# Kernel tuning notes

Measured on AMD Instinct MI355X. Metric: run time of the kernel, lower is better.

## Reference

```python
import jax, jax.numpy as jnp
import numpy as np

K_MASK = -2.3819763e38  # gemma masking constant


def apply_rope(inputs, positions, head_dim):
    # inputs: [B, T, N, H], positions: [B, T]
    half = head_dim // 2
    fraction = 2.0 * jnp.arange(half, dtype=jnp.float32) / head_dim
    timescale = 10000.0 ** fraction                      # [half]
    sinusoid = positions[..., None].astype(jnp.float32) / timescale  # [B, T, half]
    sin = jnp.sin(sinusoid)[:, :, None, :]               # [B, T, 1, half]
    cos = jnp.cos(sinusoid)[:, :, None, :]
    first, second = jnp.split(inputs, 2, axis=-1)
    out = jnp.concatenate([first * cos - second * sin,
                           second * cos + first * sin], axis=-1)
    return out.astype(inputs.dtype)


def setup_inputs() -> dict:
    key = jax.random.key(0)
    k0, k1, k2, k3 = jax.random.split(key, 4)
    B, T, D, N, H = 4, 1024, 2048, 16, 128
    x = jax.random.normal(k0, (B, T, D), dtype=jnp.float32)
    wq = jax.random.normal(k1, (N, D, H), dtype=jnp.float32) * 0.02
    wkv = jax.random.normal(k2, (2, 1, D, H), dtype=jnp.float32) * 0.02  # MQA: 1 kv head
    wo = jax.random.normal(k3, (N, H, D), dtype=jnp.float32) * 0.02
    segment_pos = jnp.broadcast_to(jnp.arange(T, dtype=jnp.int32), (B, T))
    attn_mask = jnp.broadcast_to(jnp.tril(jnp.ones((T, T), dtype=bool)), (B, T, T))
    return {"x": x, "wq": wq, "wkv": wkv, "wo": wo,
            "segment_pos": segment_pos, "attn_mask": attn_mask}


def reference(x, wq, wkv, wo, segment_pos, attn_mask):
    N, _, H = wq.shape
    # projections
    q = jnp.einsum('BTD,NDH->BTNH', x, wq)          # [B,T,N,H]
    kv = jnp.einsum('BSD,CKDH->CBSKH', x, wkv)      # [2,B,S,1,H]
    k, v = kv[0], kv[1]
    # RoPE + scaling
    q = apply_rope(q, segment_pos, H) * (H ** -0.5)
    k = apply_rope(k, segment_pos, H)
    # MQA head repeat: 1 kv head -> N heads
    k = jnp.repeat(k, N, axis=-2)                   # [B,S,N,H]
    v = jnp.repeat(v, N, axis=-2)
    # attention with manual masked softmax
    logits = jnp.einsum('BTNH,BSNH->BTNS', q, k)
    padded = jnp.where(attn_mask[:, :, None, :], logits, K_MASK)
    probs = jax.nn.softmax(padded, axis=-1).astype(k.dtype)
    encoded = jnp.einsum('BTNS,BSNH->BTNH', probs, v)
    return jnp.einsum('BTNH,NHD->BTD', encoded, wo)
```

## Files before the change

kernel.cpp:

```cpp
#include <hip/hip_runtime.h>
#include <cstdint>
#include <cstddef>

typedef unsigned short u16;
typedef __attribute__((ext_vector_type(8))) short bf16x8;
typedef __attribute__((ext_vector_type(4))) float f32x4;

#define B_ 4
#define T_ 1024
#define D_ 2048
#define N_ 16
#define H_ 128
#define BT_ (B_ * T_)
#define KMASK (-2.3819763e38f)

__device__ __forceinline__ u16 f2bf(float f) {
  uint32_t u = __builtin_bit_cast(uint32_t, f);
  u += 0x7FFFu + ((u >> 16) & 1u);
  return (u16)(u >> 16);
}
__device__ __forceinline__ float bf2f(uint32_t u) {
  return __builtin_bit_cast(float, u << 16);
}

__device__ __forceinline__ void gload16(const void* g, void* l) {
  __builtin_amdgcn_global_load_lds((const __attribute__((address_space(1))) void*)g,
                                   (__attribute__((address_space(3))) void*)l, 16, 0, 0);
}

__global__ __launch_bounds__(256) void convert_x_kernel(const float* __restrict__ x,
                                                        u16* __restrict__ xb) {
  int i = (blockIdx.x * 256 + threadIdx.x) * 8;
  float4 v0 = *(const float4*)(x + i);
  float4 v1 = *(const float4*)(x + i + 4);
  uint4 o;
  o.x = (uint32_t)f2bf(v0.x) | ((uint32_t)f2bf(v0.y) << 16);
  o.y = (uint32_t)f2bf(v0.z) | ((uint32_t)f2bf(v0.w) << 16);
  o.z = (uint32_t)f2bf(v1.x) | ((uint32_t)f2bf(v1.y) << 16);
  o.w = (uint32_t)f2bf(v1.z) | ((uint32_t)f2bf(v1.w) << 16);
  *(uint4*)(xb + i) = o;
}

__global__ __launch_bounds__(256) void transpose_kernel(const float* __restrict__ src,
                                                        u16* __restrict__ dst, int R, int C) {
  __shared__ float tile[32][33];
  const int z = blockIdx.z;
  const float* s = src + (size_t)z * R * C;
  u16* d = dst + (size_t)z * R * C;
  const int tx = threadIdx.x, ty = threadIdx.y;
  const int r0 = blockIdx.y * 32, c0 = blockIdx.x * 32;
#pragma unroll
  for (int i = 0; i < 4; ++i)
    tile[ty + i * 8][tx] = s[(size_t)(r0 + ty + i * 8) * C + (c0 + tx)];
  __syncthreads();
#pragma unroll
  for (int i = 0; i < 4; ++i)
    d[(size_t)(c0 + ty + i * 8) * R + (r0 + tx)] = f2bf(tile[tx][ty + i * 8]);
}

__global__ __launch_bounds__(256) void rope_table_kernel(float* __restrict__ costab,
                                                         float* __restrict__ sintab) {
  int idx = blockIdx.x * 256 + threadIdx.x;
  int p = idx >> 6, i = idx & 63;
  float ts = powf(10000.0f, (float)i * (1.0f / 64.0f));
  float ang = (float)p / ts;
  costab[idx] = cosf(ang);
  sintab[idx] = sinf(ang);
}

__global__ __launch_bounds__(256) void proj_gemm_kernel(
    const u16* __restrict__ xb, const u16* __restrict__ wqT, const u16* __restrict__ wkvT,
    u16* __restrict__ qraw, u16* __restrict__ kraw, u16* __restrict__ vT) {
  __shared__ alignas(16) u16 a_lds[128 * 64];
  __shared__ alignas(16) u16 b_lds[128 * 64];
  const int bid = blockIdx.x;
  const int newbid = (bid & 7) * 72 + (bid >> 3);
  const int y = newbid >> 5;
  const int m0 = (newbid & 31) * 128;
  const u16* Bt = (y < N_) ? (wqT + (size_t)y * H_ * D_) : (wkvT + (size_t)(y - N_) * H_ * D_);
  const int tid = threadIdx.x;
  const int w = tid >> 6, lane = tid & 63;
  const int g = lane >> 4, li = lane & 15;
  const int mrow = (w >> 1) * 64, wc = (w & 1) * 64;
  f32x4 acc[4][4];
#pragma unroll
  for (int i = 0; i < 4; ++i)
#pragma unroll
    for (int j = 0; j < 4; ++j) acc[i][j] = (f32x4){0.f, 0.f, 0.f, 0.f};

  for (int k0 = 0; k0 < D_; k0 += 64) {
    __syncthreads();
#pragma unroll
    for (int it = 0; it < 4; ++it) {
      int chunk = it * 256 + tid;
      int row = chunk >> 3, cu = chunk & 7;
      gload16(xb + (size_t)(m0 + row) * D_ + k0 + ((cu ^ (row & 7)) << 3), &a_lds[chunk * 8]);
    }
#pragma unroll
    for (int it = 0; it < 4; ++it) {
      int chunk = it * 256 + tid;
      int row = chunk >> 3, cu = chunk & 7;
      gload16(Bt + (size_t)row * D_ + k0 + ((cu ^ (row & 7)) << 3), &b_lds[chunk * 8]);
    }
    __syncthreads();
#pragma unroll
    for (int c2 = 0; c2 < 2; ++c2) {
      bf16x8 af[4], bfr[4];
#pragma unroll
      for (int i = 0; i < 4; ++i) {
        int row = mrow + i * 16 + li;
        af[i] = *(const bf16x8*)((const char*)a_lds +
                                 row * 128 + ((c2 * 64 + g * 16) ^ ((row & 7) << 4)));
      }
#pragma unroll
      for (int j = 0; j < 4; ++j) {
        int row = wc + j * 16 + li;
        bfr[j] = *(const bf16x8*)((const char*)b_lds +
                                  row * 128 + ((c2 * 64 + g * 16) ^ ((row & 7) << 4)));
      }
#pragma unroll
      for (int i = 0; i < 4; ++i)
#pragma unroll
        for (int j = 0; j < 4; ++j)
          acc[i][j] = __builtin_amdgcn_mfma_f32_16x16x32_bf16(af[i], bfr[j], acc[i][j], 0, 0, 0);
    }
  }

  const int b = m0 >> 10;
  if (y == N_ + 1) {
    const int tbase0 = (m0 & 1023) + mrow;
#pragma unroll
    for (int i = 0; i < 4; ++i) {
      int tbase = tbase0 + i * 16 + g * 4;
#pragma unroll
      for (int j = 0; j < 4; ++j) {
        int h = wc + j * 16 + li;
        ushort4 pk;
        pk.x = f2bf(acc[i][j][0]);
        pk.y = f2bf(acc[i][j][1]);
        pk.z = f2bf(acc[i][j][2]);
        pk.w = f2bf(acc[i][j][3]);
        *(ushort4*)(vT + ((size_t)(b * H_ + h)) * T_ + tbase) = pk;
      }
    }
  } else {
    size_t rowbase = (y < N_) ? ((size_t)(b * N_ + y) * T_ + (m0 & 1023)) : (size_t)m0;
    u16* dst0 = (y < N_) ? qraw : kraw;
#pragma unroll
    for (int i = 0; i < 4; ++i)
#pragma unroll
      for (int r = 0; r < 4; ++r) {
        int trow = mrow + i * 16 + g * 4 + r;
        u16* dst = dst0 + (rowbase + trow) * H_;
#pragma unroll
        for (int j = 0; j < 4; ++j) dst[wc + j * 16 + li] = f2bf(acc[i][j][r]);
      }
  }
}

__global__ __launch_bounds__(256) void rope_apply_k_kernel(
    const u16* __restrict__ kraw, const int* __restrict__ segment_pos,
    const float* __restrict__ costab, const float* __restrict__ sintab,
    u16* __restrict__ kb) {
  const int rid = blockIdx.x * 8 + (threadIdx.x >> 5);
  const int j = threadIdx.x & 31;
  const u16* src = kraw + (size_t)rid * H_;
  u16* dst = kb + (size_t)rid * H_;
  int p = segment_pos[rid];
  p = p < 0 ? 0 : (p > 1023 ? 1023 : p);
  uint32_t ua = *(const uint32_t*)(src + 2 * j);
  uint32_t ub = *(const uint32_t*)(src + 64 + 2 * j);
  float2 cv = *(const float2*)(costab + p * 64 + 2 * j);
  float2 sv = *(const float2*)(sintab + p * 64 + 2 * j);
  float f1a = bf2f(ua & 0xffffu), f1b = bf2f(ua >> 16);
  float f2a = bf2f(ub & 0xffffu), f2b = bf2f(ub >> 16);
  *(uint32_t*)(dst + 2 * j) =
      (uint32_t)f2bf(f1a * cv.x - f2a * sv.x) | ((uint32_t)f2bf(f1b * cv.y - f2b * sv.y) << 16);
  *(uint32_t*)(dst + 64 + 2 * j) =
      (uint32_t)f2bf(f2a * cv.x + f1a * sv.x) | ((uint32_t)f2bf(f2b * cv.y + f1b * sv.y) << 16);
}

__global__ __launch_bounds__(256) void attn_kernel(
    const u16* __restrict__ qraw, const u16* __restrict__ kb, const u16* __restrict__ vT,
    const int* __restrict__ segment_pos, const float* __restrict__ costab,
    const float* __restrict__ sintab, u16* __restrict__ enc) {
  __shared__ alignas(16) u16 k_lds[2][64 * 128];
  __shared__ alignas(16) u16 v_lds[2][128 * 64];
  __shared__ alignas(16) u16 p_lds[4 * 2 * 16 * 64];
  const int bx = blockIdx.x;
  const int j = bx >> 6;
  const int bn = bx & 63;
  const int b = bn >> 4, n = bn & 15;
  const int tid = threadIdx.x, w = tid >> 6, lane = tid & 63;
  const int g = lane >> 4, li = lane & 15;
  const int t0g[2] = {j * 64 + w * 16, (15 - j) * 64 + w * 16};

  bf16x8 qf[2][4];
  const float scale = 0.08838834764831845f;
#pragma unroll
  for (int u = 0; u < 2; ++u) {
    const int trow = t0g[u] + li;
    const u16* qrow = qraw + ((size_t)(b * N_ + n) * T_ + trow) * H_;
#pragma unroll
    for (int c = 0; c < 4; ++c) qf[u][c] = *(const bf16x8*)(qrow + c * 32 + g * 8);
    int p = segment_pos[b * T_ + trow];
    p = p < 0 ? 0 : (p > 1023 ? 1023 : p);
#pragma unroll
    for (int c = 0; c < 2; ++c) {
      const float* cp = costab + p * 64 + c * 32 + g * 8;
      const float* sp = sintab + p * 64 + c * 32 + g * 8;
      f32x4 cv0 = *(const f32x4*)cp, cv1 = *(const f32x4*)(cp + 4);
      f32x4 sv0 = *(const f32x4*)sp, sv1 = *(const f32x4*)(sp + 4);
#pragma unroll
      for (int e = 0; e < 8; ++e) {
        float cvv = e < 4 ? cv0[e] : cv1[e - 4];
        float svv = e < 4 ? sv0[e] : sv1[e - 4];
        float f1 = bf2f((u16)qf[u][c][e]);
        float f2 = bf2f((u16)qf[u][c + 2][e]);
        qf[u][c][e] = (short)f2bf((f1 * cvv - f2 * svv) * scale);
        qf[u][c + 2][e] = (short)f2bf((f2 * cvv + f1 * svv) * scale);
      }
    }
  }

  f32x4 o[2][8];
#pragma unroll
  for (int u = 0; u < 2; ++u)
#pragma unroll
    for (int hn = 0; hn < 8; ++hn) o[u][hn] = (f32x4){0.f, 0.f, 0.f, 0.f};
  float m[2] = {-3e38f, -3e38f}, lsum[2] = {0.f, 0.f};

  auto stageKV = [&](int buf, int s0) {
#pragma unroll
    for (int it = 0; it < 4; ++it) {
      int chunk = it * 256 + tid;
      int row = chunk >> 4, cu = chunk & 15;
      gload16(kb + ((size_t)b * T_ + s0 + row) * H_ + ((cu ^ (row & 7)) << 3),
              &k_lds[buf][chunk * 8]);
    }
#pragma unroll
    for (int it = 0; it < 4; ++it) {
      int chunk = it * 256 + tid;
      int row = chunk >> 3, cu = chunk & 7;
      gload16(vT + ((size_t)(b * H_ + row)) * T_ + s0 + ((cu ^ (row & 7)) << 3),
              &v_lds[buf][chunk * 8]);
    }
  };

  const int nst = 16 - j;
  stageKV(0, 0);
  __syncthreads();
  int cur = 0;
  for (int st = 0; st < nst; ++st) {
    const int s0 = st * 64;
    if (st + 1 < nst) stageKV(cur ^ 1, (st + 1) * 64);
    const bool actA = (st <= j);

    f32x4 sacc[2][4];
#pragma unroll
    for (int u = 0; u < 2; ++u)
#pragma unroll
      for (int fn = 0; fn < 4; ++fn) sacc[u][fn] = (f32x4){0.f, 0.f, 0.f, 0.f};
    __builtin_amdgcn_s_setprio(1);
#pragma unroll
    for (int c = 0; c < 4; ++c) {
      bf16x8 kf[4];
#pragma unroll
      for (int fn = 0; fn < 4; ++fn) {
        int row = fn * 16 + li;
        kf[fn] = *(const bf16x8*)((const char*)&k_lds[cur][0] +
                                  row * 256 + ((c * 64 + g * 16) ^ ((row & 7) << 4)));
      }
#pragma unroll
      for (int fn = 0; fn < 4; ++fn)
        sacc[1][fn] = __builtin_amdgcn_mfma_f32_16x16x32_bf16(kf[fn], qf[1][c], sacc[1][fn], 0, 0, 0);
      if (actA)
#pragma unroll
        for (int fn = 0; fn < 4; ++fn)
          sacc[0][fn] = __builtin_amdgcn_mfma_f32_16x16x32_bf16(kf[fn], qf[0][c], sacc[0][fn], 0, 0, 0);
    }
    __builtin_amdgcn_s_setprio(0);

#pragma unroll
    for (int u = 0; u < 2; ++u) {
      if (u == 0 && !actA) continue;
      const int t0 = t0g[u];
      const bool needmask = (u == 0) ? (st == j) : (st == nst - 1);
      if (needmask) {
        int trow = t0 + li;
#pragma unroll
        for (int fn = 0; fn < 4; ++fn)
#pragma unroll
          for (int r = 0; r < 4; ++r)
            if (s0 + fn * 16 + g * 4 + r > trow) sacc[u][fn][r] = KMASK;
      }
      float mx = -3e38f;
#pragma unroll
      for (int fn = 0; fn < 4; ++fn)
#pragma unroll
        for (int r = 0; r < 4; ++r) mx = fmaxf(mx, sacc[u][fn][r]);
      mx = fmaxf(mx, __shfl_xor(mx, 16, 64));
      mx = fmaxf(mx, __shfl_xor(mx, 32, 64));
      float mn = fmaxf(m[u], mx);
      float alpha = __expf(m[u] - mn);
      m[u] = mn;
      float ps = 0.f;
#pragma unroll
      for (int fn = 0; fn < 4; ++fn)
#pragma unroll
        for (int r = 0; r < 4; ++r) {
          float p = __expf(sacc[u][fn][r] - mn);
          sacc[u][fn][r] = p;
          ps += p;
        }
      ps += __shfl_xor(ps, 16, 64);
      ps += __shfl_xor(ps, 32, 64);
      lsum[u] = lsum[u] * alpha + ps;
      char* pbase = (char*)p_lds + (w * 2 + u) * 2048;
#pragma unroll
      for (int fn = 0; fn < 4; ++fn) {
        ushort4 pk;
        pk.x = f2bf(sacc[u][fn][0]);
        pk.y = f2bf(sacc[u][fn][1]);
        pk.z = f2bf(sacc[u][fn][2]);
        pk.w = f2bf(sacc[u][fn][3]);
        *(ushort4*)(pbase + li * 128 + ((fn * 32 + g * 8) ^ ((li & 7) << 4))) = pk;
      }
#pragma unroll
      for (int r = 0; r < 4; ++r) {
        float ar = __shfl(alpha, g * 4 + r, 64);
#pragma unroll
        for (int hn = 0; hn < 8; ++hn) o[u][hn][r] *= ar;
      }
    }

    __builtin_amdgcn_s_setprio(1);
#pragma unroll
    for (int c2 = 0; c2 < 2; ++c2) {
      bf16x8 pfB = *(const bf16x8*)((char*)p_lds + (w * 2 + 1) * 2048 + li * 128 +
                                    ((c2 * 64 + g * 16) ^ ((li & 7) << 4)));
      bf16x8 pfA;
      if (actA)
        pfA = *(const bf16x8*)((char*)p_lds + (w * 2 + 0) * 2048 + li * 128 +
                               ((c2 * 64 + g * 16) ^ ((li & 7) << 4)));
#pragma unroll
      for (int hn = 0; hn < 8; ++hn) {
        int hrow = hn * 16 + li;
        bf16x8 vf = *(const bf16x8*)((const char*)&v_lds[cur][0] +
                                     hrow * 128 + ((c2 * 64 + g * 16) ^ ((li & 7) << 4)));
        o[1][hn] = __builtin_amdgcn_mfma_f32_16x16x32_bf16(pfB, vf, o[1][hn], 0, 0, 0);
        if (actA)
          o[0][hn] = __builtin_amdgcn_mfma_f32_16x16x32_bf16(pfA, vf, o[0][hn], 0, 0, 0);
      }
    }
    __builtin_amdgcn_s_setprio(0);
    __syncthreads();
    cur ^= 1;
  }

#pragma unroll
  for (int u = 0; u < 2; ++u)
#pragma unroll
    for (int r = 0; r < 4; ++r) {
      float lr = __shfl(lsum[u], g * 4 + r, 64);
      float inv = 1.0f / lr;
      int t = t0g[u] + g * 4 + r;
      u16* dst = enc + ((size_t)(b * T_ + t)) * (N_ * H_) + n * H_;
#pragma unroll
      for (int hn = 0; hn < 8; ++hn) dst[hn * 16 + li] = f2bf(o[u][hn][r] * inv);
    }
}

__global__ __launch_bounds__(256) void out_gemm_kernel(const u16* __restrict__ enc,
                                                       const u16* __restrict__ woT,
                                                       float* __restrict__ out) {
  __shared__ alignas(16) u16 a_lds[128 * 64];
  __shared__ alignas(16) u16 b_lds[128 * 64];
  const int bid = blockIdx.x;
  const int newbid = (bid & 7) * 64 + (bid >> 3);
  const int m0 = (newbid & 31) * 128;
  const int n0 = (newbid >> 5) * 128;
  const int tid = threadIdx.x, w = tid >> 6, lane = tid & 63;
  const int g = lane >> 4, li = lane & 15;
  const int mrow = (w >> 1) * 64, wc = (w & 1) * 64;
  f32x4 acc[4][4];
#pragma unroll
  for (int i = 0; i < 4; ++i)
#pragma unroll
    for (int j = 0; j < 4; ++j) acc[i][j] = (f32x4){0.f, 0.f, 0.f, 0.f};

  for (int k0 = 0; k0 < D_; k0 += 64) {
    __syncthreads();
#pragma unroll
    for (int it = 0; it < 4; ++it) {
      int chunk = it * 256 + tid;
      int row = chunk >> 3, cu = chunk & 7;
      gload16(enc + (size_t)(m0 + row) * D_ + k0 + ((cu ^ (row & 7)) << 3), &a_lds[chunk * 8]);
    }
#pragma unroll
    for (int it = 0; it < 4; ++it) {
      int chunk = it * 256 + tid;
      int row = chunk >> 3, cu = chunk & 7;
      gload16(woT + (size_t)(n0 + row) * D_ + k0 + ((cu ^ (row & 7)) << 3), &b_lds[chunk * 8]);
    }
    __syncthreads();
#pragma unroll
    for (int c2 = 0; c2 < 2; ++c2) {
      bf16x8 af[4], bfr[4];
#pragma unroll
      for (int i = 0; i < 4; ++i) {
        int row = mrow + i * 16 + li;
        af[i] = *(const bf16x8*)((const char*)a_lds +
                                 row * 128 + ((c2 * 64 + g * 16) ^ ((row & 7) << 4)));
      }
#pragma unroll
      for (int j = 0; j < 4; ++j) {
        int row = wc + j * 16 + li;
        bfr[j] = *(const bf16x8*)((const char*)b_lds +
                                  row * 128 + ((c2 * 64 + g * 16) ^ ((row & 7) << 4)));
      }
#pragma unroll
      for (int i = 0; i < 4; ++i)
#pragma unroll
        for (int j = 0; j < 4; ++j)
          acc[i][j] = __builtin_amdgcn_mfma_f32_16x16x32_bf16(af[i], bfr[j], acc[i][j], 0, 0, 0);
    }
  }
#pragma unroll
  for (int i = 0; i < 4; ++i)
#pragma unroll
    for (int r = 0; r < 4; ++r) {
      int bt = m0 + mrow + i * 16 + g * 4 + r;
      float* dst = out + (size_t)bt * D_ + n0 + wc;
#pragma unroll
      for (int j = 0; j < 4; ++j) dst[j * 16 + li] = acc[i][j][r];
    }
}

extern "C" void kernel_launch(void* const* d_in, const int* in_sizes, int n_in,
                              void* d_out, int out_size, void* d_ws, size_t ws_size,
                              hipStream_t stream) {
  const float* x = (const float*)d_in[0];
  const float* wq = (const float*)d_in[1];
  const float* wkv = (const float*)d_in[2];
  const float* wo = (const float*)d_in[3];
  const int* segment_pos = (const int*)d_in[4];
  float* out = (float*)d_out;

  char* ws = (char*)d_ws;
  size_t off = 0;
  auto alloc = [&](size_t bytes) -> void* {
    void* p = ws + off;
    off += (bytes + 255) & ~(size_t)255;
    return p;
  };
  u16* xb   = (u16*)alloc((size_t)BT_ * D_ * 2);
  u16* wqT  = (u16*)alloc((size_t)N_ * H_ * D_ * 2);
  u16* wkvT = (u16*)alloc((size_t)2 * H_ * D_ * 2);
  u16* woT  = (u16*)alloc((size_t)D_ * N_ * H_ * 2);
  u16* qraw = (u16*)alloc((size_t)B_ * N_ * T_ * H_ * 2);
  u16* kb   = (u16*)alloc((size_t)B_ * T_ * H_ * 2);
  u16* kraw = (u16*)alloc((size_t)B_ * T_ * H_ * 2);
  u16* vT   = (u16*)alloc((size_t)B_ * H_ * T_ * 2);
  u16* enc  = (u16*)alloc((size_t)BT_ * N_ * H_ * 2);
  float* costab = (float*)alloc(1024 * 64 * 4);
  float* sintab = (float*)alloc(1024 * 64 * 4);

  convert_x_kernel<<<BT_ * D_ / 8 / 256, 256, 0, stream>>>(x, xb);
  dim3 tb(32, 8);
  transpose_kernel<<<dim3(H_ / 32, D_ / 32, N_), tb, 0, stream>>>(wq, wqT, D_, H_);
  transpose_kernel<<<dim3(H_ / 32, D_ / 32, 2), tb, 0, stream>>>(wkv, wkvT, D_, H_);
  transpose_kernel<<<dim3(D_ / 32, D_ / 32, 1), tb, 0, stream>>>(wo, woT, N_ * H_, D_);
  rope_table_kernel<<<256, 256, 0, stream>>>(costab, sintab);
  proj_gemm_kernel<<<576, 256, 0, stream>>>(xb, wqT, wkvT, qraw, kraw, vT);
  rope_apply_k_kernel<<<BT_ / 8, 256, 0, stream>>>(kraw, segment_pos, costab, sintab, kb);
  attn_kernel<<<512, 256, 0, stream>>>(qraw, kb, vT, segment_pos, costab, sintab, enc);
  out_gemm_kernel<<<512, 256, 0, stream>>>(enc, woT, out);
}
```

Baseline: 201.5 us.

## Use exp2 softmax with lazy rescale, direct V loads, packed bf16 convert

Folds log2(e) into the query scale so the softmax can use exp2f. It skips the running-max rescale of the accumulator unless some row's max grows by more than a threshold. V is no longer staged through LDS. Each wave reads V fragments straight from global memory into registers before the PV MFMAs, which frees LDS so launch bounds can request 3 blocks per CU. Probability packing now uses the v_cvt_pk_bf16_f32 instruction. The risks are exposed global load latency in the PV loop, redundant V reads across waves, and bounded but larger intermediate exponent values.

```diff
diff --git a/kernel.cpp b/kernel.cpp
--- a/kernel.cpp
+++ b/kernel.cpp
@@ -180,12 +180,11 @@
       (uint32_t)f2bf(f2a * cv.x + f1a * sv.x) | ((uint32_t)f2bf(f2b * cv.y + f1b * sv.y) << 16);
 }
 
-__global__ __launch_bounds__(256) void attn_kernel(
+__global__ __launch_bounds__(256, 3) void attn_kernel(
     const u16* __restrict__ qraw, const u16* __restrict__ kb, const u16* __restrict__ vT,
     const int* __restrict__ segment_pos, const float* __restrict__ costab,
     const float* __restrict__ sintab, u16* __restrict__ enc) {
   __shared__ alignas(16) u16 k_lds[2][64 * 128];
-  __shared__ alignas(16) u16 v_lds[2][128 * 64];
   __shared__ alignas(16) u16 p_lds[4 * 2 * 16 * 64];
   const int bx = blockIdx.x;
   const int j = bx >> 6;
@@ -196,7 +195,7 @@
   const int t0g[2] = {j * 64 + w * 16, (15 - j) * 64 + w * 16};
 
   bf16x8 qf[2][4];
-  const float scale = 0.08838834764831845f;
+  const float scale = 0.12751743342f;
 #pragma unroll
   for (int u = 0; u < 2; ++u) {
     const int trow = t0g[u] + li;
@@ -230,7 +229,7 @@
     for (int hn = 0; hn < 8; ++hn) o[u][hn] = (f32x4){0.f, 0.f, 0.f, 0.f};
   float m[2] = {-3e38f, -3e38f}, lsum[2] = {0.f, 0.f};
 
-  auto stageKV = [&](int buf, int s0) {
+  auto stageK = [&](int buf, int s0) {
 #pragma unroll
     for (int it = 0; it < 4; ++it) {
       int chunk = it * 256 + tid;
@@ -238,22 +237,15 @@
       gload16(kb + ((size_t)b * T_ + s0 + row) * H_ + ((cu ^ (row & 7)) << 3),
               &k_lds[buf][chunk * 8]);
     }
-#pragma unroll
-    for (int it = 0; it < 4; ++it) {
-      int chunk = it * 256 + tid;
-      int row = chunk >> 3, cu = chunk & 7;
-      gload16(vT + ((size_t)(b * H_ + row)) * T_ + s0 + ((cu ^ (row & 7)) << 3),
-              &v_lds[buf][chunk * 8]);
-    }
   };
 
   const int nst = 16 - j;
-  stageKV(0, 0);
+  stageK(0, 0);
   __syncthreads();
   int cur = 0;
   for (int st = 0; st < nst; ++st) {
     const int s0 = st * 64;
-    if (st + 1 < nst) stageKV(cur ^ 1, (st + 1) * 64);
+    if (st + 1 < nst) stageK(cur ^ 1, (st + 1) * 64);
     const bool actA = (st <= j);
 
     f32x4 sacc[2][4];
@@ -301,42 +293,51 @@
         for (int r = 0; r < 4; ++r) mx = fmaxf(mx, sacc[u][fn][r]);
       mx = fmaxf(mx, __shfl_xor(mx, 16, 64));
       mx = fmaxf(mx, __shfl_xor(mx, 32, 64));
-      float mn = fmaxf(m[u], mx);
-      float alpha = __expf(m[u] - mn);
-      m[u] = mn;
+      if (__any(mx - m[u] > 11.5f)) {
+        float mn = fmaxf(m[u], mx);
+        float alpha = exp2f(m[u] - mn);
+        m[u] = mn;
+        lsum[u] *= alpha;
+#pragma unroll
+        for (int r = 0; r < 4; ++r) {
+          float ar = __shfl(alpha, g * 4 + r, 64);
+#pragma unroll
+          for (int hn = 0; hn < 8; ++hn) o[u][hn][r] *= ar;
+        }
+      }
       float ps = 0.f;
 #pragma unroll
       for (int fn = 0; fn < 4; ++fn)
 #pragma unroll
         for (int r = 0; r < 4; ++r) {
-          float p = __expf(sacc[u][fn][r] - mn);
+          float p = exp2f(sacc[u][fn][r] - m[u]);
           sacc[u][fn][r] = p;
           ps += p;
         }
       ps += __shfl_xor(ps, 16, 64);
       ps += __shfl_xor(ps, 32, 64);
-      lsum[u] = lsum[u] * alpha + ps;
+      lsum[u] += ps;
       char* pbase = (char*)p_lds + (w * 2 + u) * 2048;
 #pragma unroll
       for (int fn = 0; fn < 4; ++fn) {
-        ushort4 pk;
-        pk.x = f2bf(sacc[u][fn][0]);
-        pk.y = f2bf(sacc[u][fn][1]);
-        pk.z = f2bf(sacc[u][fn][2]);
-        pk.w = f2bf(sacc[u][fn][3]);
-        *(ushort4*)(pbase + li * 128 + ((fn * 32 + g * 8) ^ ((li & 7) << 4))) = pk;
-      }
-#pragma unroll
-      for (int r = 0; r < 4; ++r) {
-        float ar = __shfl(alpha, g * 4 + r, 64);
-#pragma unroll
-        for (int hn = 0; hn < 8; ++hn) o[u][hn][r] *= ar;
+        uint32_t w0, w1;
+        asm("v_cvt_pk_bf16_f32 %0, %1, %2"
+            : "=v"(w0) : "v"(sacc[u][fn][0]), "v"(sacc[u][fn][1]));
+        asm("v_cvt_pk_bf16_f32 %0, %1, %2"
+            : "=v"(w1) : "v"(sacc[u][fn][2]), "v"(sacc[u][fn][3]));
+        uint2 pk2 = {w0, w1};
+        *(uint2*)(pbase + li * 128 + ((fn * 32 + g * 8) ^ ((li & 7) << 4))) = pk2;
       }
     }
 
     __builtin_amdgcn_s_setprio(1);
 #pragma unroll
     for (int c2 = 0; c2 < 2; ++c2) {
+      bf16x8 vfr[8];
+#pragma unroll
+      for (int hn = 0; hn < 8; ++hn)
+        vfr[hn] =
+            *(const bf16x8*)(vT + ((size_t)(b * H_ + hn * 16 + li)) * T_ + s0 + c2 * 32 + g * 8);
       bf16x8 pfB = *(const bf16x8*)((char*)p_lds + (w * 2 + 1) * 2048 + li * 128 +
                                     ((c2 * 64 + g * 16) ^ ((li & 7) << 4)));
       bf16x8 pfA;
@@ -345,12 +346,9 @@
                                ((c2 * 64 + g * 16) ^ ((li & 7) << 4)));
 #pragma unroll
       for (int hn = 0; hn < 8; ++hn) {
-        int hrow = hn * 16 + li;
-        bf16x8 vf = *(const bf16x8*)((const char*)&v_lds[cur][0] +
-                                     hrow * 128 + ((c2 * 64 + g * 16) ^ ((li & 7) << 4)));
-        o[1][hn] = __builtin_amdgcn_mfma_f32_16x16x32_bf16(pfB, vf, o[1][hn], 0, 0, 0);
+        o[1][hn] = __builtin_amdgcn_mfma_f32_16x16x32_bf16(pfB, vfr[hn], o[1][hn], 0, 0, 0);
         if (actA)
-          o[0][hn] = __builtin_amdgcn_mfma_f32_16x16x32_bf16(pfA, vf, o[0][hn], 0, 0, 0);
+          o[0][hn] = __builtin_amdgcn_mfma_f32_16x16x32_bf16(pfA, vfr[hn], o[0][hn], 0, 0, 0);
       }
     }
     __builtin_amdgcn_s_setprio(0);
```

Measured after the change: 313.0 us. 1.55x slower.
